# Kernel optimization log

Measured on AMD Instinct MI355X. Metric: run time of the kernel, lower is better.

The kernel has to match this reference:

```python
import jax, jax.numpy as jnp
import numpy as np

B, L, V, D, H = 64, 128, 20000, 300, 256
NE, NA = 34, 36  # num_events, num_arguments


def _param(key, shape, scale=0.05):
    return (jax.random.normal(key, shape, dtype=jnp.float32) * scale)


def setup_inputs() -> dict:
    key = jax.random.key(0)
    ks = jax.random.split(key, 16)
    inp = {
        "emb_table": _param(ks[0], (V, D)),
        # PyTorch LSTM layout: gates stacked [i, f, g, o] -> [4H, in]
        "W_ih_f": _param(ks[1], (4 * H, D)),
        "W_hh_f": _param(ks[2], (4 * H, H)),
        "b_ih_f": _param(ks[3], (4 * H,)),
        "b_hh_f": _param(ks[4], (4 * H,)),
        "W_ih_b": _param(ks[5], (4 * H, D)),
        "W_hh_b": _param(ks[6], (4 * H, H)),
        "b_ih_b": _param(ks[7], (4 * H,)),
        "b_hh_b": _param(ks[8], (4 * H,)),
        "W_ev": _param(ks[9], (NE, 2 * H + NE - 1)),
        "b_ev": _param(ks[10], (NE,)),
        "W_arg": _param(ks[11], (NA, 4 * H)),
        "b_arg": _param(ks[12], (NA,)),
        "input_ids": jax.random.randint(ks[13], (B, L), 0, V, dtype=jnp.int32),
    }
    return inp


def _lstm_dir(x_pre, W_hh, reverse):
    # x_pre: [L, B, 4H] precomputed input projection (+ biases)
    Bsz = x_pre.shape[1]
    h0 = jnp.zeros((Bsz, H), dtype=x_pre.dtype)
    c0 = jnp.zeros((Bsz, H), dtype=x_pre.dtype)

    def cell(carry, p):
        h, c = carry
        gates = p + h @ W_hh.T
        i, f, g, o = jnp.split(gates, 4, axis=-1)
        i = jax.nn.sigmoid(i)
        f = jax.nn.sigmoid(f)
        g = jnp.tanh(g)
        o = jax.nn.sigmoid(o)
        c = f * c + i * g
        h = o * jnp.tanh(c)
        return (h, c), h

    _, hs = jax.lax.scan(cell, (h0, c0), x_pre, reverse=reverse)
    return hs  # [L, B, H]


def reference(emb_table, W_ih_f, W_hh_f, b_ih_f, b_hh_f,
              W_ih_b, W_hh_b, b_ih_b, b_hh_b,
              W_ev, b_ev, W_arg, b_arg, input_ids):
    # Embedding lookup: [B, L, D]
    emb = emb_table[input_ids]

    # BiLSTM. Precompute input projections once per direction.
    x = jnp.transpose(emb, (1, 0, 2))  # [L, B, D]
    pre_f = jnp.einsum('lbd,gd->lbg', x, W_ih_f) + b_ih_f + b_hh_f
    pre_b = jnp.einsum('lbd,gd->lbg', x, W_ih_b) + b_ih_b + b_hh_b
    h_f = _lstm_dir(pre_f, W_hh_f, reverse=False)
    h_b = _lstm_dir(pre_b, W_hh_b, reverse=True)
    hs = jnp.concatenate([h_f, h_b], axis=-1)  # [L, B, 2H]

    # --- Event head: sequential scan over time with g_trg state ---
    def step(g_trg, h_t):
        # h_t: [B, 2H]; g_trg: [B, NE-1] (0/1 flags, detached w.r.t. grads)
        feat = jnp.concatenate([h_t, g_trg], axis=1)
        logit = feat @ W_ev.T + b_ev  # [B, NE]  (dropout is identity in eval)
        pred = jnp.argmax(logit, axis=-1)  # [B]
        upd = (pred > 0).astype(logit.dtype)
        oh = jax.nn.one_hot(jnp.maximum(pred - 1, 0), NE - 1,
                            dtype=logit.dtype) * upd[:, None]
        g_trg = jnp.maximum(g_trg, oh)  # scatter-set 1 at pred-1 where pred>0
        return g_trg, logit

    g0 = jnp.zeros((hs.shape[1], NE - 1), dtype=hs.dtype)
    _, ev = jax.lax.scan(step, g0, hs)
    event_logits = jnp.transpose(ev, (1, 0, 2))  # [B, L, NE]

    # --- Argument head: independent of g_trg, vectorize over trigger i ---
    # arguments_logits[b, i, j] = W_arg @ concat(h[b, j], h[b, i]) + b_arg
    h_blc = jnp.transpose(hs, (1, 0, 2))  # [B, L, 2H]
    Wj = W_arg[:, :2 * H]  # acts on per-position hidden h[b, j]
    Wi = W_arg[:, 2 * H:]  # acts on broadcast trigger hidden h[b, i]
    part_j = jnp.einsum('bld,ad->bla', h_blc, Wj)  # [B, L, NA]
    part_i = jnp.einsum('bld,ad->bla', h_blc, Wi)  # [B, L, NA]
    arguments_logits = (part_i[:, :, None, :] + part_j[:, None, :, :]
                        + b_arg)  # [B, L(trigger), L(token), NA]

    return event_logits, arguments_logits
```

## Files before the change

kernel.cpp:

```cpp
#include <hip/hip_runtime.h>
#include <cstddef>
#include <cmath>

#define B_    64
#define L_    128
#define V_    20000
#define D_    300
#define H_    256
#define NE_   34
#define NA_   36
#define M_    8192
#define KP_   304
#define NPROJ_ 2048
#define K2_   512
#define NCAT_ 128

__device__ __forceinline__ float sigmoidf_(float x) { return 1.0f / (1.0f + expf(-x)); }

typedef __attribute__((ext_vector_type(2))) _Float16 half2_;

__device__ __forceinline__ half2_ u2h(unsigned u) {
    union { unsigned u; half2_ h; } c; c.u = u; return c.h;
}
__device__ __forceinline__ unsigned packh2(float a, float b) {
    union { half2_ h; unsigned u; } c;
    c.h = half2_{(_Float16)a, (_Float16)b};
    return c.u;
}

#if __has_builtin(__builtin_amdgcn_fdot2)
__device__ __forceinline__ float fdot2_(half2_ a, half2_ b, float c) {
    return __builtin_amdgcn_fdot2(a, b, c, false);
}
#else
__device__ __forceinline__ float fdot2_(half2_ a, half2_ b, float c) {
    return c + (float)a.x * (float)b.x + (float)a.y * (float)b.y;
}
#endif

__global__ __launch_bounds__(256) void k_gather(const float* __restrict__ emb,
                                                const int* __restrict__ ids,
                                                float* __restrict__ X) {
    int idx = blockIdx.x * 256 + threadIdx.x;
    if (idx >= M_ * KP_) return;
    int m = idx / KP_, k = idx - m * KP_;
    int l = m >> 6, b = m & 63;
    float v = 0.f;
    if (k < D_) {
        int tok = ids[b * L_ + l];
        v = emb[(size_t)tok * D_ + k];
    }
    X[idx] = v;
}

__global__ __launch_bounds__(256) void k_prep_wih(const float* __restrict__ Wf,
                                                  const float* __restrict__ Wb,
                                                  const float* __restrict__ bihf,
                                                  const float* __restrict__ bhhf,
                                                  const float* __restrict__ bihb,
                                                  const float* __restrict__ bhhb,
                                                  float* __restrict__ Wt,
                                                  float* __restrict__ bias) {
    int idx = blockIdx.x * 256 + threadIdx.x;
    if (idx >= KP_ * NPROJ_) return;
    int k = idx / NPROJ_, n = idx - k * NPROJ_;
    int dir = n >> 10, g = n & 1023;
    float v = 0.f;
    if (k < D_) v = dir ? Wb[g * D_ + k] : Wf[g * D_ + k];
    Wt[idx] = v;
    if (k == 0) bias[n] = dir ? (bihb[g] + bhhb[g]) : (bihf[g] + bhhf[g]);
}

__global__ __launch_bounds__(256) void k_prep_whh16(const float* __restrict__ Wf,
                                                    const float* __restrict__ Wb,
                                                    unsigned* __restrict__ Wp) {
    int idx = blockIdx.x * 256 + threadIdx.x;
    if (idx >= 2 * 128 * 1024) return;
    int dir = idx >> 17, r = idx & 131071;
    int j = r >> 12;
    int g = (r >> 2) & 1023;
    int c = r & 3;
    int kp = (j << 2) | c;
    const float* W = dir ? Wb : Wf;
    Wp[idx] = packh2(W[g * H_ + 2 * kp], W[g * H_ + 2 * kp + 1]);
}

__global__ __launch_bounds__(256) void k_prep_wcat(const float* __restrict__ Warg,
                                                   const float* __restrict__ Wev,
                                                   const float* __restrict__ barg,
                                                   const float* __restrict__ bev,
                                                   float* __restrict__ Wcat,
                                                   float* __restrict__ bias) {
    int idx = blockIdx.x * 256 + threadIdx.x;
    if (idx >= K2_ * NCAT_) return;
    int k = idx >> 7, n = idx & 127;
    float v = 0.f;
    if (n < 36)       v = Warg[n * 1024 + k];
    else if (n < 72)  v = Warg[(n - 36) * 1024 + 512 + k];
    else if (n < 106) v = Wev[(n - 72) * 545 + k];
    Wcat[idx] = v;
    if (k == 0) {
        float bv = 0.f;
        if (n >= 36 && n < 72)       bv = barg[n - 36];
        else if (n >= 72 && n < 106) bv = bev[n - 72];
        bias[n] = bv;
    }
}

template <int K>
__global__ __launch_bounds__(256) void k_gemm(const float* __restrict__ A,
                                              const float* __restrict__ Bm,
                                              const float* __restrict__ bias,
                                              float* __restrict__ C, int N) {
    __shared__ float As[16][64];
    __shared__ float Bs[16][64];
    const int tid = threadIdx.x;
    const int m0 = blockIdx.x * 64, n0 = blockIdx.y * 64;
    const int tx = tid & 15, ty = tid >> 4;
    const int a_m = tid >> 2;
    const int a_k = (tid & 3) << 2;
    const int b_k = tid >> 4;
    const int b_n = (tid & 15) << 2;

    float acc[4][4] = {};
    for (int k0 = 0; k0 < K; k0 += 16) {
        float4 av = *(const float4*)&A[(size_t)(m0 + a_m) * K + k0 + a_k];
        float4 bv = *(const float4*)&Bm[(size_t)(k0 + b_k) * N + n0 + b_n];
        __syncthreads();
        As[a_k][a_m] = av.x; As[a_k + 1][a_m] = av.y;
        As[a_k + 2][a_m] = av.z; As[a_k + 3][a_m] = av.w;
        *(float4*)&Bs[b_k][b_n] = bv;
        __syncthreads();
#pragma unroll
        for (int kk = 0; kk < 16; kk++) {
            float4 a4 = *(const float4*)&As[kk][ty << 2];
            float4 b4 = *(const float4*)&Bs[kk][tx << 2];
            float ar[4] = {a4.x, a4.y, a4.z, a4.w};
            float br[4] = {b4.x, b4.y, b4.z, b4.w};
#pragma unroll
            for (int i = 0; i < 4; i++)
#pragma unroll
                for (int j = 0; j < 4; j++) acc[i][j] += ar[i] * br[j];
        }
    }
    float4 bb = *(const float4*)&bias[n0 + (tx << 2)];
#pragma unroll
    for (int i = 0; i < 4; i++) {
        int m = m0 + (ty << 2) + i;
        float4 o;
        o.x = acc[i][0] + bb.x; o.y = acc[i][1] + bb.y;
        o.z = acc[i][2] + bb.z; o.w = acc[i][3] + bb.w;
        *(float4*)&C[(size_t)m * N + n0 + (tx << 2)] = o;
    }
}

__global__ __launch_bounds__(1024) void k_lstm6(const float* __restrict__ pre,
                                                const unsigned* __restrict__ Wp,
                                                float* __restrict__ hs) {
    __shared__ float pbuf[1024];
    __shared__ __align__(16) unsigned h2s[128];

    const int blk = blockIdx.x;
    const int dir = blk >> 6;
    const int b   = blk & 63;
    const int g   = threadIdx.x;
    const int tid = threadIdx.x;

    const uint4* Wr4 = (const uint4*)Wp;
    uint4 w[32];
#pragma unroll
    for (int j = 0; j < 32; ++j)
        w[j] = Wr4[(size_t)((dir << 5) + j) * 1024 + g];
    if (tid < 128) h2s[tid] = 0u;
    __syncthreads();

    const uint4* h2s4 = (const uint4*)h2s;
    float c_state = 0.f;

    for (int step = 0; step < L_; ++step) {
        const int l = dir ? (L_ - 1 - step) : step;

        float acc = pre[((size_t)(l * B_ + b) << 11) + (dir << 10) + g];
#pragma unroll
        for (int j = 0; j < 32; ++j) {
            uint4 h4 = h2s4[j];
            acc = fdot2_(u2h(w[j].x), u2h(h4.x), acc);
            acc = fdot2_(u2h(w[j].y), u2h(h4.y), acc);
            acc = fdot2_(u2h(w[j].z), u2h(h4.z), acc);
            acc = fdot2_(u2h(w[j].w), u2h(h4.w), acc);
        }
        pbuf[g] = acc;
        __syncthreads();

        if (tid < 256) {
            const int u = tid;
            float ig = sigmoidf_(pbuf[u]);
            float fg = sigmoidf_(pbuf[256 + u]);
            float gg = tanhf(pbuf[512 + u]);
            float og = sigmoidf_(pbuf[768 + u]);
            float c = fg * c_state + ig * gg;
            c_state = c;
            float h = og * tanhf(c);
            hs[((size_t)(l * B_ + b) << 9) + (dir << 8) + u] = h;
            float hn = __shfl_xor(h, 1, 64);
            if (!(u & 1)) h2s[u >> 1] = packh2(h, hn);
        }
        __syncthreads();
    }
}

__global__ __launch_bounds__(64) void k_event(const float* __restrict__ part,
                                              const float* __restrict__ Wev,
                                              float* __restrict__ out_ev) {
    const int b = blockIdx.x;
    const int e = threadIdx.x;
    __shared__ float sg[33];
    if (e < 33) sg[e] = 0.f;
    float wreg[33];
    if (e < NE_) {
#pragma unroll
        for (int j = 0; j < 33; j++) wreg[j] = Wev[e * 545 + 512 + j];
    }
    __syncthreads();
    for (int l = 0; l < L_; l++) {
        const int m = l * B_ + b;
        float v = -3.0e38f;
        if (e < NE_) {
            v = part[(size_t)m * NCAT_ + 72 + e];
#pragma unroll
            for (int j = 0; j < 33; j++) v += wreg[j] * sg[j];
            out_ev[((size_t)b * L_ + l) * NE_ + e] = v;
        }
        float bv = v;
        int bi = e;
#pragma unroll
        for (int off = 32; off > 0; off >>= 1) {
            float ov = __shfl_xor(bv, off, 64);
            int oi = __shfl_xor(bi, off, 64);
            if (ov > bv || (ov == bv && oi < bi)) { bv = ov; bi = oi; }
        }
        __syncthreads();
        if (bi > 0 && e == bi - 1) sg[e] = 1.f;
        __syncthreads();
    }
}

__global__ __launch_bounds__(256) void k_arg(const float* __restrict__ part,
                                             float* __restrict__ out) {
    const int blk = blockIdx.x;
    const int b = blk >> 7, i = blk & 127;
    __shared__ float pj[L_ * NA_];
    __shared__ float pi_s[NA_];
    const int tid = threadIdx.x;
    if (tid < NA_) pi_s[tid] = part[(size_t)(i * B_ + b) * NCAT_ + 36 + tid];
    for (int idx = tid; idx < L_ * NA_; idx += 256) {
        int j = idx / NA_, a = idx - j * NA_;
        pj[idx] = part[(size_t)(j * B_ + b) * NCAT_ + a];
    }
    __syncthreads();
    float* o = out + (size_t)blk * (L_ * NA_);
    for (int idx = tid; idx < L_ * NA_; idx += 256) {
        int a = idx % NA_;
        o[idx] = pi_s[a] + pj[idx];
    }
}

extern "C" void kernel_launch(void* const* d_in, const int* in_sizes, int n_in,
                              void* d_out, int out_size, void* d_ws, size_t ws_size,
                              hipStream_t stream) {
    const float* emb  = (const float*)d_in[0];
    const float* Wihf = (const float*)d_in[1];
    const float* Whhf = (const float*)d_in[2];
    const float* bihf = (const float*)d_in[3];
    const float* bhhf = (const float*)d_in[4];
    const float* Wihb = (const float*)d_in[5];
    const float* Whhb = (const float*)d_in[6];
    const float* bihb = (const float*)d_in[7];
    const float* bhhb = (const float*)d_in[8];
    const float* Wev  = (const float*)d_in[9];
    const float* bev  = (const float*)d_in[10];
    const float* Warg = (const float*)d_in[11];
    const float* barg = (const float*)d_in[12];
    const int*   ids  = (const int*)d_in[13];
    float* out = (float*)d_out;
    float* ws  = (float*)d_ws;

    float*    X       = ws;
    float*    part    = ws;
    float*    Wt_ih   = ws + 2490368;
    float*    bias_p  = ws + 3112960;
    unsigned* Wp16    = (unsigned*)(ws + 3115008);
    float*    Wcat    = ws + 3639296;
    float*    bias_c  = ws + 3704832;
    float*    pre_all = ws + 3704960;
    float*    hsbuf   = ws + 20482176;

    k_gather<<<(M_ * KP_) / 256, 256, 0, stream>>>(emb, ids, X);
    k_prep_wih<<<(KP_ * NPROJ_) / 256, 256, 0, stream>>>(Wihf, Wihb, bihf, bhhf, bihb, bhhb, Wt_ih, bias_p);
    k_prep_whh16<<<(2 * 128 * 1024) / 256, 256, 0, stream>>>(Whhf, Whhb, Wp16);
    k_prep_wcat<<<(K2_ * NCAT_) / 256, 256, 0, stream>>>(Warg, Wev, barg, bev, Wcat, bias_c);

    k_gemm<KP_><<<dim3(M_ / 64, NPROJ_ / 64), 256, 0, stream>>>(X, Wt_ih, bias_p, pre_all, NPROJ_);
    k_lstm6<<<128, 1024, 0, stream>>>(pre_all, Wp16, hsbuf);
    k_gemm<K2_><<<dim3(M_ / 64, NCAT_ / 64), 256, 0, stream>>>(hsbuf, Wcat, bias_c, part, NCAT_);
    k_event<<<B_, 64, 0, stream>>>(part, Wev, out);
    k_arg<<<B_ * L_, 256, 0, stream>>>(part, out + (size_t)B_ * L_ * NE_);
}
```

Measured before the change: 971.0 us.

## Split LSTM recurrent weights between registers and LDS with 512-thread blocks

The recurrent LSTM kernel drops from 1024 to 512 threads per block, and each thread now computes two gate rows. Each thread holds 24 of the 32 fp16 weight chunks in registers and reads the remaining 8 from a 128KB dynamic LDS buffer. The aim is to cut per-thread register pressure and wave count per step while keeping the whole W_hh slice on-chip. In exchange it adds LDS read traffic every timestep, and it needs a one-time host attribute call to raise the dynamic shared memory limit.

```diff
diff --git a/kernel.cpp b/kernel.cpp
--- a/kernel.cpp
+++ b/kernel.cpp
@@ -14,6 +14,9 @@
 #define NPROJ_ 2048
 #define K2_   512
 #define NCAT_ 128
+
+#define JREG_ 24
+#define JLDS_ 8
 
 __device__ __forceinline__ float sigmoidf_(float x) { return 1.0f / (1.0f + expf(-x)); }
 
@@ -154,23 +157,35 @@
     }
 }
 
-__global__ __launch_bounds__(1024) void k_lstm6(const float* __restrict__ pre,
-                                                const unsigned* __restrict__ Wp,
-                                                float* __restrict__ hs) {
-    __shared__ float pbuf[1024];
-    __shared__ __align__(16) unsigned h2s[128];
+__global__ __launch_bounds__(512, 2) void k_lstm7(const float* __restrict__ pre,
+                                                  const unsigned* __restrict__ Wp,
+                                                  float* __restrict__ hs) {
+    extern __shared__ __align__(16) char smem7[];
+    uint4*    WL4  = (uint4*)smem7;
+    float*    pbuf = (float*)(smem7 + 131072);
+    unsigned* h2s  = (unsigned*)(smem7 + 131072 + 4096);
 
     const int blk = blockIdx.x;
     const int dir = blk >> 6;
     const int b   = blk & 63;
-    const int g   = threadIdx.x;
     const int tid = threadIdx.x;
-
-    const uint4* Wr4 = (const uint4*)Wp;
-    uint4 w[32];
-#pragma unroll
-    for (int j = 0; j < 32; ++j)
-        w[j] = Wr4[(size_t)((dir << 5) + j) * 1024 + g];
+    const int g0  = tid;
+    const int g1  = tid + 512;
+
+    const uint4* Wr4 = (const uint4*)Wp + ((size_t)dir << 15);
+
+    for (int it = 0; it < 16; ++it) {
+        int i2 = tid + (it << 9);
+        int j  = i2 >> 10;
+        int g  = i2 & 1023;
+        WL4[(j << 10) + g] = Wr4[(size_t)(JREG_ + j) * 1024 + g];
+    }
+    uint4 w0[JREG_], w1[JREG_];
+#pragma unroll
+    for (int j = 0; j < JREG_; ++j) {
+        w0[j] = Wr4[(size_t)j * 1024 + g0];
+        w1[j] = Wr4[(size_t)j * 1024 + g1];
+    }
     if (tid < 128) h2s[tid] = 0u;
     __syncthreads();
 
@@ -179,17 +194,38 @@
 
     for (int step = 0; step < L_; ++step) {
         const int l = dir ? (L_ - 1 - step) : step;
-
-        float acc = pre[((size_t)(l * B_ + b) << 11) + (dir << 10) + g];
-#pragma unroll
-        for (int j = 0; j < 32; ++j) {
+        const float* p = pre + ((size_t)(l * B_ + b) << 11) + (dir << 10);
+        float acc0 = p[g0];
+        float acc1 = p[g1];
+
+#pragma unroll
+        for (int j = 0; j < JREG_; ++j) {
             uint4 h4 = h2s4[j];
-            acc = fdot2_(u2h(w[j].x), u2h(h4.x), acc);
-            acc = fdot2_(u2h(w[j].y), u2h(h4.y), acc);
-            acc = fdot2_(u2h(w[j].z), u2h(h4.z), acc);
-            acc = fdot2_(u2h(w[j].w), u2h(h4.w), acc);
-        }
-        pbuf[g] = acc;
+            acc0 = fdot2_(u2h(w0[j].x), u2h(h4.x), acc0);
+            acc0 = fdot2_(u2h(w0[j].y), u2h(h4.y), acc0);
+            acc0 = fdot2_(u2h(w0[j].z), u2h(h4.z), acc0);
+            acc0 = fdot2_(u2h(w0[j].w), u2h(h4.w), acc0);
+            acc1 = fdot2_(u2h(w1[j].x), u2h(h4.x), acc1);
+            acc1 = fdot2_(u2h(w1[j].y), u2h(h4.y), acc1);
+            acc1 = fdot2_(u2h(w1[j].z), u2h(h4.z), acc1);
+            acc1 = fdot2_(u2h(w1[j].w), u2h(h4.w), acc1);
+        }
+#pragma unroll
+        for (int j = 0; j < JLDS_; ++j) {
+            uint4 h4 = h2s4[JREG_ + j];
+            uint4 wa = WL4[(j << 10) + g0];
+            uint4 wb = WL4[(j << 10) + g1];
+            acc0 = fdot2_(u2h(wa.x), u2h(h4.x), acc0);
+            acc0 = fdot2_(u2h(wa.y), u2h(h4.y), acc0);
+            acc0 = fdot2_(u2h(wa.z), u2h(h4.z), acc0);
+            acc0 = fdot2_(u2h(wa.w), u2h(h4.w), acc0);
+            acc1 = fdot2_(u2h(wb.x), u2h(h4.x), acc1);
+            acc1 = fdot2_(u2h(wb.y), u2h(h4.y), acc1);
+            acc1 = fdot2_(u2h(wb.z), u2h(h4.z), acc1);
+            acc1 = fdot2_(u2h(wb.w), u2h(h4.w), acc1);
+        }
+        pbuf[g0] = acc0;
+        pbuf[g1] = acc1;
         __syncthreads();
 
         if (tid < 256) {
@@ -295,13 +331,20 @@
     float*    pre_all = ws + 3704960;
     float*    hsbuf   = ws + 20482176;
 
+    static bool s_attr_done = false;
+    if (!s_attr_done) {
+        (void)hipFuncSetAttribute(reinterpret_cast<const void*>(k_lstm7),
+                                  hipFuncAttributeMaxDynamicSharedMemorySize, 135680);
+        s_attr_done = true;
+    }
+
     k_gather<<<(M_ * KP_) / 256, 256, 0, stream>>>(emb, ids, X);
     k_prep_wih<<<(KP_ * NPROJ_) / 256, 256, 0, stream>>>(Wihf, Wihb, bihf, bhhf, bihb, bhhb, Wt_ih, bias_p);
     k_prep_whh16<<<(2 * 128 * 1024) / 256, 256, 0, stream>>>(Whhf, Whhb, Wp16);
     k_prep_wcat<<<(K2_ * NCAT_) / 256, 256, 0, stream>>>(Warg, Wev, barg, bev, Wcat, bias_c);
 
     k_gemm<KP_><<<dim3(M_ / 64, NPROJ_ / 64), 256, 0, stream>>>(X, Wt_ih, bias_p, pre_all, NPROJ_);
-    k_lstm6<<<128, 1024, 0, stream>>>(pre_all, Wp16, hsbuf);
+    k_lstm7<<<128, 512, 135680, stream>>>(pre_all, Wp16, hsbuf);
     k_gemm<K2_><<<dim3(M_ / 64, NCAT_ / 64), 256, 0, stream>>>(hsbuf, Wcat, bias_c, part, NCAT_);
     k_event<<<B_, 64, 0, stream>>>(part, Wev, out);
     k_arg<<<B_ * L_, 256, 0, stream>>>(part, out + (size_t)B_ * L_ * NE_);
```

Result: faster. 796.4 us (-18.0%).
